# Kernel optimization log

Measured on AMD Instinct MI355X. Metric: run time of the kernel, lower is better.

Reference implementation:

```python
import jax, jax.numpy as jnp
import numpy as np

B, N, D = 2, 2048, 1024
H = 16
HD = D // H  # 64
SCALE = 8.0 / HD  # muP scale = 0.125
EPS = 1e-5


def setup_inputs() -> dict:
    key = jax.random.key(0)
    ks = jax.random.split(key, 7)
    s = 0.02  # realistic init scale for weights
    return {
        "xq": jax.random.normal(ks[0], (B, N, D), jnp.float32),
        "xk": jax.random.normal(ks[1], (B, N, D), jnp.float32),
        "xv": jax.random.normal(ks[2], (B, N, D), jnp.float32),
        "wq": jax.random.normal(ks[3], (D, D), jnp.float32) * s,
        "wk": jax.random.normal(ks[4], (D, D), jnp.float32) * s,
        "wv": jax.random.normal(ks[5], (D, D), jnp.float32) * s,
        "wproj": jax.random.normal(ks[6], (D, D), jnp.float32) * s,
    }


def _layernorm_noaffine(x):
    # Fp32LayerNorm over last dim, no bias / no affine params
    x32 = x.astype(jnp.float32)
    mu = jnp.mean(x32, axis=-1, keepdims=True)
    var = jnp.mean(jnp.square(x32 - mu), axis=-1, keepdims=True)
    return ((x32 - mu) * jax.lax.rsqrt(var + EPS)).astype(x.dtype)


def _heads(x):
    # [B, N, H*HD] -> [B, H, N, HD]
    b, n, _ = x.shape
    return x.reshape(b, n, H, HD).transpose(0, 2, 1, 3)


def reference(xq, xk, xv, wq, wk, wv, wproj):
    # nn.Linear: y = x @ W^T (no bias)
    q = _heads(xq @ wq.T)
    k = _heads(xk @ wk.T)
    v = _heads(xv @ wv.T)
    q = _layernorm_noaffine(q)
    k = _layernorm_noaffine(k)
    # dense attention (score_mod=None, block_mask=None), muP scale
    scores = jnp.einsum("bhqd,bhkd->bhqk", q, k) * SCALE
    attn = jax.nn.softmax(scores, axis=-1)
    o = jnp.einsum("bhqk,bhkd->bhqd", attn, v)
    o = o.transpose(0, 2, 1, 3).reshape(xq.shape[0], xq.shape[1], D)
    return o @ wproj.T
```

## Files before the change

kernel.cpp:

```cpp
#include <hip/hip_runtime.h>

typedef __bf16 bf16x8 __attribute__((ext_vector_type(8)));
typedef float f32x4 __attribute__((ext_vector_type(4)));
typedef float f32x16 __attribute__((ext_vector_type(16)));
typedef unsigned u32x4 __attribute__((ext_vector_type(4)));

#define DEV __device__ __forceinline__
#define L2E 1.44269504f

DEV unsigned short f2bf(float f) {
  unsigned u = __float_as_uint(f);
  u += 0x7fffu + ((u >> 16) & 1u);
  return (unsigned short)(u >> 16);
}
DEV float bf2f(unsigned short h) { return __uint_as_float(((unsigned)h) << 16); }

DEV void gload16(const void* g, void* l) {
  __builtin_amdgcn_global_load_lds((const __attribute__((address_space(1))) void*)g,
                                   (__attribute__((address_space(3))) void*)l, 16, 0, 0);
}

DEV unsigned cvtpk2(float lo, float hi) {
  unsigned r;
  asm("v_cvt_pk_bf16_f32 %0, %1, %2" : "=v"(r) : "v"(lo), "v"(hi));
  return r;
}
DEV void plswap(unsigned& a, unsigned& b) {
  asm volatile("v_permlane32_swap_b32 %0, %1" : "+v"(a), "+v"(b));
}
DEV float ex2(float x) {
  float r;
  asm("v_exp_f32 %0, %1" : "=v"(r) : "v"(x));
  return r;
}
DEV float max3(float a, float b, float c) {
  float r;
  asm("v_max3_f32 %0, %1, %2, %3" : "=v"(r) : "v"(a), "v"(b), "v"(c));
  return r;
}

__global__ __launch_bounds__(256) void cvt7(const float* xq, const float* xk, const float* xv,
                                            const float* wq, const float* wk, const float* wv,
                                            const float* wp, ushort4* xqb, ushort4* xkb,
                                            ushort4* xvb, ushort4* wqb, ushort4* wkb,
                                            ushort4* wvb, ushort4* wpb, int nx4, int nw4) {
  const int y = blockIdx.y;
  const float4* s;
  ushort4* d;
  int n;
  switch (y) {
    case 0: s = (const float4*)xq; d = xqb; n = nx4; break;
    case 1: s = (const float4*)xk; d = xkb; n = nx4; break;
    case 2: s = (const float4*)xv; d = xvb; n = nx4; break;
    case 3: s = (const float4*)wq; d = wqb; n = nw4; break;
    case 4: s = (const float4*)wk; d = wkb; n = nw4; break;
    case 5: s = (const float4*)wv; d = wvb; n = nw4; break;
    default: s = (const float4*)wp; d = wpb; n = nw4; break;
  }
  for (int i = blockIdx.x * 256 + threadIdx.x; i < n; i += gridDim.x * 256) {
    float4 v = s[i];
    ushort4 o;
    o.x = f2bf(v.x); o.y = f2bf(v.y); o.z = f2bf(v.z); o.w = f2bf(v.w);
    d[i] = o;
  }
}

template <bool SWAP>
DEV void gemm_core(const unsigned short* __restrict__ A, const unsigned short* __restrict__ W,
                   char* sA, char* sB, f32x4 acc[4][4], int bm, int bn, int tid) {
  const int w = tid >> 6, lane = tid & 63;
  const int wm = w >> 1, wn = w & 1;
  const char* aB = (const char*)A + ((size_t)(bm * 128 + (lane >> 3)) << 11) +
                   (((lane & 7) ^ (lane >> 3)) << 4);
  const char* bB = (const char*)W + ((size_t)(bn * 128 + (lane >> 3)) << 11) +
                   (((lane & 7) ^ (lane >> 3)) << 4);
  const int ldsBase = w * 1024;

  for (int kt = 0; kt < 16; ++kt) {
    const int ko = kt * 128;
#pragma unroll
    for (int c = 0; c < 4; ++c) {
      gload16(aB + ((size_t)(c * 32 + w * 8) << 11) + ko, sA + c * 4096 + ldsBase);
      gload16(bB + ((size_t)(c * 32 + w * 8) << 11) + ko, sB + c * 4096 + ldsBase);
    }
    __syncthreads();
#pragma unroll
    for (int kk = 0; kk < 2; ++kk) {
      const int ch = ((kk * 4 + (lane >> 4)) ^ (lane & 7)) << 4;
      bf16x8 aF[4], bF[4];
#pragma unroll
      for (int mi = 0; mi < 4; ++mi)
        aF[mi] = *(const bf16x8*)(sA + (wm * 64 + mi * 16 + (lane & 15)) * 128 + ch);
#pragma unroll
      for (int ni = 0; ni < 4; ++ni)
        bF[ni] = *(const bf16x8*)(sB + (wn * 64 + ni * 16 + (lane & 15)) * 128 + ch);
#pragma unroll
      for (int mi = 0; mi < 4; ++mi)
#pragma unroll
        for (int ni = 0; ni < 4; ++ni)
          acc[mi][ni] = SWAP ? __builtin_amdgcn_mfma_f32_16x16x32_bf16(bF[ni], aF[mi],
                                                                       acc[mi][ni], 0, 0, 0)
                             : __builtin_amdgcn_mfma_f32_16x16x32_bf16(aF[mi], bF[ni],
                                                                       acc[mi][ni], 0, 0, 0);
    }
    __syncthreads();
  }
}

__global__ __launch_bounds__(256, 3) void gemm_qkv(
    const unsigned short* __restrict__ xq, const unsigned short* __restrict__ xk,
    const unsigned short* __restrict__ xv, const unsigned short* __restrict__ wq,
    const unsigned short* __restrict__ wk, const unsigned short* __restrict__ wv,
    unsigned short* __restrict__ qh, unsigned short* __restrict__ kh,
    unsigned short* __restrict__ vt) {
  __shared__ char sA[16384], sB[16384];
  const int z = blockIdx.z;
  const int flat = blockIdx.x + (blockIdx.y << 3);
  const int xcd = flat & 7, ii = flat >> 3;
  const int bm = xcd * 4 + (ii >> 3), bn = ii & 7;
  const int tid = threadIdx.x, w = tid >> 6, lane = tid & 63;
  const int wm = w >> 1, wn = w & 1;

  if (z == 2) {
    f32x4 acc[4][4];
#pragma unroll
    for (int i = 0; i < 4; ++i)
#pragma unroll
      for (int j = 0; j < 4; ++j) acc[i][j] = (f32x4){0.f, 0.f, 0.f, 0.f};
    gemm_core<false>(xv, wv, sA, sB, acc, bm, bn, tid);
    const int hb = bn * 2 + wn;
    const int d = (lane & 15);
    const int g0 = bm * 128 + wm * 64 + ((lane >> 4) << 2);
#pragma unroll
    for (int mi = 0; mi < 4; ++mi) {
      const int g = g0 + mi * 16;
      const int b = g >> 11, n0 = g & 2047, tq = n0 >> 6, nn = n0 & 63;
#pragma unroll
      for (int ni = 0; ni < 4; ++ni) {
        const int dd = d + ni * 16;
        char* dst = (char*)vt + (((size_t)((b * 16 + hb) * 32 + tq) * 64 + dd) << 7) +
                    ((nn * 2) ^ ((dd & 7) << 4));
        *(uint2*)dst = make_uint2(cvtpk2(acc[mi][ni][0], acc[mi][ni][1]),
                                  cvtpk2(acc[mi][ni][2], acc[mi][ni][3]));
      }
    }
  } else {
    const unsigned short* A = z == 0 ? xq : xk;
    const unsigned short* W = z == 0 ? wq : wk;
    f32x4 acc[4][4];
#pragma unroll
    for (int i = 0; i < 4; ++i)
#pragma unroll
      for (int j = 0; j < 4; ++j) acc[i][j] = (f32x4){0.f, 0.f, 0.f, 0.f};
    gemm_core<true>(A, W, sA, sB, acc, bm, bn, tid);
    unsigned short* dst = z == 0 ? qh : kh;
    const float osc = z == 0 ? 0.125f * L2E : 1.0f;
    const int h = bn * 2 + wn;
    const int d0b = (lane >> 4) << 3;
#pragma unroll
    for (int mi = 0; mi < 4; ++mi) {
      float s = 0.f, ss = 0.f;
#pragma unroll
      for (int ni = 0; ni < 4; ++ni)
#pragma unroll
        for (int r = 0; r < 4; ++r) {
          const float v = acc[mi][ni][r];
          s += v;
          ss += v * v;
        }
      s += __shfl_xor(s, 16); ss += __shfl_xor(ss, 16);
      s += __shfl_xor(s, 32); ss += __shfl_xor(ss, 32);
      const float mean = s * 0.015625f;
      const float var = ss * 0.015625f - mean * mean;
      const float rstd = rsqrtf(var + 1e-5f) * osc;
      const float mr = mean * rstd;
      const int g = bm * 128 + wm * 64 + mi * 16 + (lane & 15);
      const int b = g >> 11, n = g & 2047;
      const int bh = b * 16 + h, tq = n >> 6, rr = n & 63;
      char* rowp = (char*)dst + (((size_t)(bh * 32 + tq) * 64 + rr) << 7);
      const int swz = (rr & 7) << 4;
#pragma unroll
      for (int ni = 0; ni < 4; ++ni) {
        const unsigned u0 = cvtpk2(fmaf(acc[mi][ni][0], rstd, -mr), fmaf(acc[mi][ni][1], rstd, -mr));
        const unsigned u1 = cvtpk2(fmaf(acc[mi][ni][2], rstd, -mr), fmaf(acc[mi][ni][3], rstd, -mr));
        *(uint2*)(rowp + ((ni * 32 + d0b) ^ swz)) = make_uint2(u0, u1);
      }
    }
  }
}

__global__ __launch_bounds__(256, 3) void gemm_out(const unsigned short* __restrict__ A,
                                                   const unsigned short* __restrict__ Wp,
                                                   float* __restrict__ C) {
  __shared__ char sA[16384], sB[8192];
  const int flat = blockIdx.x + (blockIdx.y << 4);
  const int xcd = flat & 7, ii = flat >> 3;
  const int bm = xcd * 4 + (ii & 3), bn = ii >> 2;
  const int tid = threadIdx.x, w = tid >> 6, lane = tid & 63;
  const int wm = w >> 1, wn = w & 1;
  f32x4 acc[4][2];
#pragma unroll
  for (int i = 0; i < 4; ++i)
#pragma unroll
    for (int j = 0; j < 2; ++j) acc[i][j] = (f32x4){0.f, 0.f, 0.f, 0.f};

  const char* aB = (const char*)A + ((size_t)(bm * 128 + (lane >> 3)) << 11) +
                   (((lane & 7) ^ (lane >> 3)) << 4);
  const char* bB = (const char*)Wp + ((size_t)(bn * 64 + (lane >> 3)) << 11) +
                   (((lane & 7) ^ (lane >> 3)) << 4);
  const int ldsBase = w * 1024;
  for (int kt = 0; kt < 16; ++kt) {
    const int ko = kt * 128;
#pragma unroll
    for (int c = 0; c < 4; ++c)
      gload16(aB + ((size_t)(c * 32 + w * 8) << 11) + ko, sA + c * 4096 + ldsBase);
#pragma unroll
    for (int c = 0; c < 2; ++c)
      gload16(bB + ((size_t)(c * 32 + w * 8) << 11) + ko, sB + c * 4096 + ldsBase);
    __syncthreads();
#pragma unroll
    for (int kk = 0; kk < 2; ++kk) {
      const int ch = ((kk * 4 + (lane >> 4)) ^ (lane & 7)) << 4;
      bf16x8 aF[4], bF[2];
#pragma unroll
      for (int mi = 0; mi < 4; ++mi)
        aF[mi] = *(const bf16x8*)(sA + (wm * 64 + mi * 16 + (lane & 15)) * 128 + ch);
#pragma unroll
      for (int ni = 0; ni < 2; ++ni)
        bF[ni] = *(const bf16x8*)(sB + (wn * 32 + ni * 16 + (lane & 15)) * 128 + ch);
#pragma unroll
      for (int mi = 0; mi < 4; ++mi)
#pragma unroll
        for (int ni = 0; ni < 2; ++ni)
          acc[mi][ni] = __builtin_amdgcn_mfma_f32_16x16x32_bf16(bF[ni], aF[mi], acc[mi][ni], 0, 0, 0);
    }
    __syncthreads();
  }
  const int m0 = bm * 128 + wm * 64 + (lane & 15);
  const int nb = bn * 64 + wn * 32 + ((lane >> 4) << 2);
#pragma unroll
  for (int mi = 0; mi < 4; ++mi)
#pragma unroll
    for (int ni = 0; ni < 2; ++ni) {
      const f32x4 v = acc[mi][ni];
      *(float4*)&C[(size_t)(m0 + mi * 16) * 1024 + nb + ni * 16] =
          make_float4(v[0], v[1], v[2], v[3]);
    }
}

__global__ __launch_bounds__(256, 4) void attn_fused(
    const unsigned short* __restrict__ Qp, const unsigned short* __restrict__ Kp,
    const unsigned short* __restrict__ Vp, unsigned short* __restrict__ Opart,
    float2* __restrict__ ML) {
  const int bid = blockIdx.x;
  const int xcd = bid & 7, idx = bid >> 3;
  const int bh = ((idx & 3) << 3) | xcd;
  const int quarter = (idx >> 2) & 3;
  const int qt = idx >> 4;
  __shared__ char sK[2][8192];
  __shared__ char sV[2][8192];
  const int tid = threadIdx.x, w = tid >> 6, lane = tid & 63;
  const int q5 = lane & 31, hi = lane >> 5;

  const char* qg = (const char*)Qp + ((size_t)bh * 32 + qt * 2) * 8192;
  const char* kg = (const char*)Kp + ((size_t)bh * 32 + quarter * 8) * 8192;
  const char* vg = (const char*)Vp + ((size_t)bh * 32 + quarter * 8) * 8192;

#pragma unroll
  for (int t = 0; t < 4; ++t)
    gload16(qg + (w * 4 + t) * 1024 + lane * 16, (char*)sK + (w * 4 + t) * 1024);
  __syncthreads();
  bf16x8 qf[4];
  {
    const int r128 = w * 32 + q5, tt = r128 >> 6, r = r128 & 63;
#pragma unroll
    for (int dc = 0; dc < 4; ++dc) {
      const int cb = dc * 32 + hi * 16;
      qf[dc] = *(const bf16x8*)((const char*)sK + tt * 8192 + r * 128 + (cb ^ ((r & 7) << 4)));
    }
  }
  __syncthreads();

#pragma unroll
  for (int t = 0; t < 2; ++t) {
    gload16(kg + (w * 2 + t) * 1024 + lane * 16, &sK[0][(w * 2 + t) * 1024]);
    gload16(vg + (w * 2 + t) * 1024 + lane * 16, &sV[0][(w * 2 + t) * 1024]);
  }

  f32x16 o0 = {0,0,0,0,0,0,0,0,0,0,0,0,0,0,0,0};
  f32x16 o1 = {0,0,0,0,0,0,0,0,0,0,0,0,0,0,0,0};
  float m = -1e30f, l = 0.f;

  for (int kt = 0; kt < 8; ++kt) {
    const int cur = kt & 1;
    __syncthreads();
    if (kt < 7) {
#pragma unroll
      for (int t = 0; t < 2; ++t) {
        gload16(kg + (size_t)(kt + 1) * 8192 + (w * 2 + t) * 1024 + lane * 16,
                &sK[cur ^ 1][(w * 2 + t) * 1024]);
        gload16(vg + (size_t)(kt + 1) * 8192 + (w * 2 + t) * 1024 + lane * 16,
                &sV[cur ^ 1][(w * 2 + t) * 1024]);
      }
    }
    f32x16 s0 = {0,0,0,0,0,0,0,0,0,0,0,0,0,0,0,0};
    f32x16 s1 = {0,0,0,0,0,0,0,0,0,0,0,0,0,0,0,0};
    __builtin_amdgcn_s_setprio(1);
#pragma unroll
    for (int dc = 0; dc < 4; ++dc) {
      const int cb = dc * 32 + hi * 16;
      const int ra = q5, rb = 32 + q5;
      bf16x8 kf0 = *(const bf16x8*)(&sK[cur][ra * 128 + (cb ^ ((ra & 7) << 4))]);
      bf16x8 kf1 = *(const bf16x8*)(&sK[cur][rb * 128 + (cb ^ ((rb & 7) << 4))]);
      s0 = __builtin_amdgcn_mfma_f32_32x32x16_bf16(kf0, qf[dc], s0, 0, 0, 0);
      s1 = __builtin_amdgcn_mfma_f32_32x32x16_bf16(kf1, qf[dc], s1, 0, 0, 0);
    }
    __builtin_amdgcn_s_setprio(0);
    float tt[12];
#pragma unroll
    for (int r = 0; r < 10; ++r) {
      const float a = (3 * r) < 16 ? s0[(3 * r) & 15] : s1[(3 * r) & 15];
      const float b = (3 * r + 1) < 16 ? s0[(3 * r + 1) & 15] : s1[(3 * r + 1) & 15];
      const float c = (3 * r + 2) < 16 ? s0[(3 * r + 2) & 15] : s1[(3 * r + 2) & 15];
      tt[r] = max3(a, b, c);
    }
    tt[10] = s1[14]; tt[11] = s1[15];
    tt[0] = max3(tt[0], tt[1], tt[2]);
    tt[1] = max3(tt[3], tt[4], tt[5]);
    tt[2] = max3(tt[6], tt[7], tt[8]);
    tt[3] = max3(tt[9], tt[10], tt[11]);
    const float loc = fmaxf(max3(tt[0], tt[1], tt[2]), tt[3]);
    const float mx = fmaxf(loc, __shfl_xor(loc, 32));
    if (__any(mx > m + 8.f)) {
      const float mn = fmaxf(m, mx);
      const float corr = ex2(m - mn);
      l *= corr;
#pragma unroll
      for (int r = 0; r < 16; ++r) { o0[r] *= corr; o1[r] *= corr; }
      m = mn;
    }
    const float nm = -m;
    unsigned pk[4][4];
    float rs = 0.f;
#define DO_CHUNK(c, SV, B)                                      \
  {                                                             \
    float p0 = ex2(SV[B + 0] + nm);                             \
    float p1 = ex2(SV[B + 1] + nm);                             \
    float p2 = ex2(SV[B + 2] + nm);                             \
    float p3 = ex2(SV[B + 3] + nm);                             \
    float p4 = ex2(SV[B + 4] + nm);                             \
    float p5 = ex2(SV[B + 5] + nm);                             \
    float p6 = ex2(SV[B + 6] + nm);                             \
    float p7 = ex2(SV[B + 7] + nm);                             \
    rs += ((p0 + p1) + (p2 + p3)) + ((p4 + p5) + (p6 + p7));    \
    unsigned a0 = cvtpk2(p0, p1), a1 = cvtpk2(p2, p3);          \
    unsigned b0 = cvtpk2(p4, p5), b1 = cvtpk2(p6, p7);          \
    plswap(a0, b0);                                             \
    plswap(a1, b1);                                             \
    pk[c][0] = a0; pk[c][1] = a1; pk[c][2] = b0; pk[c][3] = b1; \
  }
    DO_CHUNK(0, s0, 0)
    DO_CHUNK(1, s0, 8)
    DO_CHUNK(2, s1, 0)
    DO_CHUNK(3, s1, 8)
#undef DO_CHUNK
    rs += __shfl_xor(rs, 32);
    l += rs;
    __builtin_amdgcn_s_setprio(1);
#pragma unroll
    for (int kk = 0; kk < 4; ++kk) {
      const int cb = kk * 32 + hi * 16;
      const int ra = q5, rb = 32 + q5;
      bf16x8 vf0 = *(const bf16x8*)(&sV[cur][ra * 128 + (cb ^ ((ra & 7) << 4))]);
      bf16x8 vf1 = *(const bf16x8*)(&sV[cur][rb * 128 + (cb ^ ((rb & 7) << 4))]);
      u32x4 pw = {pk[kk][0], pk[kk][1], pk[kk][2], pk[kk][3]};
      bf16x8 pb = __builtin_bit_cast(bf16x8, pw);
      o0 = __builtin_amdgcn_mfma_f32_32x32x16_bf16(vf0, pb, o0, 0, 0, 0);
      o1 = __builtin_amdgcn_mfma_f32_32x32x16_bf16(vf1, pb, o1, 0, 0, 0);
    }
    __builtin_amdgcn_s_setprio(0);
  }

  const float invl = 1.f / l;
  const int q = qt * 128 + w * 32 + q5;
  const size_t prow = (size_t)(quarter * 32 + bh) * 2048 + q;
  unsigned short* ob = Opart + prow * 64;
#pragma unroll
  for (int g = 0; g < 4; ++g) {
    unsigned d0 = cvtpk2(o0[4 * g + 0] * invl, o0[4 * g + 1] * invl);
    unsigned d1 = cvtpk2(o0[4 * g + 2] * invl, o0[4 * g + 3] * invl);
    *(uint2*)(ob + 8 * g + 4 * hi) = make_uint2(d0, d1);
    unsigned e0 = cvtpk2(o1[4 * g + 0] * invl, o1[4 * g + 1] * invl);
    unsigned e1 = cvtpk2(o1[4 * g + 2] * invl, o1[4 * g + 3] * invl);
    *(uint2*)(ob + 32 + 8 * g + 4 * hi) = make_uint2(e0, e1);
  }
  if (hi == 0) ML[prow] = make_float2(m, l);
}

__global__ __launch_bounds__(256) void attn_merge(const unsigned short* __restrict__ Op,
                                                  const float2* __restrict__ ML,
                                                  unsigned short* __restrict__ O) {
  const int gid = blockIdx.x * 256 + threadIdx.x;
  const int row = gid >> 3, sub = gid & 7;
  float2 ml[4];
  float mm = -1e30f;
#pragma unroll
  for (int p = 0; p < 4; ++p) {
    ml[p] = ML[p * 65536 + row];
    mm = fmaxf(mm, ml[p].x);
  }
  float wgt[4], wsum = 0.f;
#pragma unroll
  for (int p = 0; p < 4; ++p) {
    wgt[p] = ml[p].y * ex2(ml[p].x - mm);
    wsum += wgt[p];
  }
  const float inv = 1.f / wsum;
  float r[8] = {0.f, 0.f, 0.f, 0.f, 0.f, 0.f, 0.f, 0.f};
#pragma unroll
  for (int p = 0; p < 4; ++p) {
    const uint4 a = *(const uint4*)(Op + ((size_t)(p * 65536) + row) * 64 + sub * 8);
    const unsigned av[4] = {a.x, a.y, a.z, a.w};
#pragma unroll
    for (int j = 0; j < 4; ++j) {
      r[2 * j] += wgt[p] * bf2f((unsigned short)(av[j] & 0xffff));
      r[2 * j + 1] += wgt[p] * bf2f((unsigned short)(av[j] >> 16));
    }
  }
  unsigned ov[4];
#pragma unroll
  for (int j = 0; j < 4; ++j)
    ov[j] = cvtpk2(r[2 * j] * inv, r[2 * j + 1] * inv);
  const int bh = row >> 11, q = row & 2047, bb = bh >> 4, h = bh & 15;
  *(uint4*)(O + ((size_t)(bb * 2048 + q) * 1024 + h * 64 + sub * 8)) =
      make_uint4(ov[0], ov[1], ov[2], ov[3]);
}

extern "C" void kernel_launch(void* const* d_in, const int* in_sizes, int n_in,
                              void* d_out, int out_size, void* d_ws, size_t ws_size,
                              hipStream_t stream) {
  const float* xq = (const float*)d_in[0];
  const float* xk = (const float*)d_in[1];
  const float* xv = (const float*)d_in[2];
  const float* wq = (const float*)d_in[3];
  const float* wk = (const float*)d_in[4];
  const float* wv = (const float*)d_in[5];
  const float* wp = (const float*)d_in[6];

  const size_t NX = 4194304;
  const size_t NW = 1048576;
  unsigned short* base = (unsigned short*)d_ws;
  unsigned short* xqb = base;
  unsigned short* xkb = base + NX;
  unsigned short* xvb = base + 2 * NX;
  unsigned short* wqb = base + 3 * NX;
  unsigned short* wkb = wqb + NW;
  unsigned short* wvb = wkb + NW;
  unsigned short* wpb = base + 3 * NX + 4 * NW;
  unsigned short* qh = wpb + NW;
  unsigned short* kh = qh + NX;
  unsigned short* vt = kh + NX;
  unsigned short* obf = vt + NX;
  float2* ml = (float2*)(obf + NX);
  unsigned short* opart = base;

  cvt7<<<dim3(512, 7), 256, 0, stream>>>(xq, xk, xv, wq, wk, wv, wp, (ushort4*)xqb,
                                         (ushort4*)xkb, (ushort4*)xvb, (ushort4*)wqb,
                                         (ushort4*)wkb, (ushort4*)wvb, (ushort4*)wpb,
                                         (int)(NX / 4), (int)(NW / 4));

  gemm_qkv<<<dim3(8, 32, 3), 256, 0, stream>>>(xqb, xkb, xvb, wqb, wkb, wvb, qh, kh, vt);

  attn_fused<<<2048, 256, 0, stream>>>(qh, kh, vt, opart, ml);
  attn_merge<<<2048, 256, 0, stream>>>(opart, ml, obf);

  gemm_out<<<dim3(16, 32), 256, 0, stream>>>(obf, wpb, (float*)d_out);
}
```

Measured before the change: 129.1 us.

## Double attention query tile per block and swap K/V fragment loads via permlane

```diff
diff --git a/kernel.cpp b/kernel.cpp
--- a/kernel.cpp
+++ b/kernel.cpp
@@ -37,6 +37,18 @@
   float r;
   asm("v_max3_f32 %0, %1, %2, %3" : "=v"(r) : "v"(a), "v"(b), "v"(c));
   return r;
+}
+
+DEV void read2swap(const char* base, int c0, int lane, bf16x8& f0, bf16x8& f1) {
+  const int swz = (lane & 7) << 4;
+  const u32x4 a = *(const u32x4*)(base + lane * 128 + (c0 ^ swz));
+  const u32x4 b = *(const u32x4*)(base + lane * 128 + ((c0 + 16) ^ swz));
+  unsigned a0 = a[0], a1 = a[1], a2 = a[2], a3 = a[3];
+  unsigned b0 = b[0], b1 = b[1], b2 = b[2], b3 = b[3];
+  plswap(a0, b0); plswap(a1, b1); plswap(a2, b2); plswap(a3, b3);
+  const u32x4 ra = {a0, a1, a2, a3}, rb = {b0, b1, b2, b3};
+  f0 = __builtin_bit_cast(bf16x8, ra);
+  f1 = __builtin_bit_cast(bf16x8, rb);
 }
 
 __global__ __launch_bounds__(256) void cvt7(const float* xq, const float* xk, const float* xv,
@@ -248,153 +260,178 @@
     }
 }
 
-__global__ __launch_bounds__(256, 4) void attn_fused(
+__global__ __launch_bounds__(256, 2) void attn_fused(
     const unsigned short* __restrict__ Qp, const unsigned short* __restrict__ Kp,
     const unsigned short* __restrict__ Vp, unsigned short* __restrict__ Opart,
     float2* __restrict__ ML) {
   const int bid = blockIdx.x;
   const int xcd = bid & 7, idx = bid >> 3;
   const int bh = ((idx & 3) << 3) | xcd;
-  const int quarter = (idx >> 2) & 3;
-  const int qt = idx >> 4;
-  __shared__ char sK[2][8192];
-  __shared__ char sV[2][8192];
+  const int rest = idx >> 2;
+  const int quarter = rest & 3;
+  const int qt = rest >> 2;
+  __shared__ char smem[32768];
   const int tid = threadIdx.x, w = tid >> 6, lane = tid & 63;
   const int q5 = lane & 31, hi = lane >> 5;
 
-  const char* qg = (const char*)Qp + ((size_t)bh * 32 + qt * 2) * 8192;
+  const char* qg = (const char*)Qp + ((size_t)bh * 32 + qt * 4) * 8192;
   const char* kg = (const char*)Kp + ((size_t)bh * 32 + quarter * 8) * 8192;
   const char* vg = (const char*)Vp + ((size_t)bh * 32 + quarter * 8) * 8192;
 
 #pragma unroll
-  for (int t = 0; t < 4; ++t)
-    gload16(qg + (w * 4 + t) * 1024 + lane * 16, (char*)sK + (w * 4 + t) * 1024);
+  for (int t = 0; t < 8; ++t)
+    gload16(qg + (w * 8 + t) * 1024 + lane * 16, smem + (w * 8 + t) * 1024);
   __syncthreads();
-  bf16x8 qf[4];
-  {
-    const int r128 = w * 32 + q5, tt = r128 >> 6, r = r128 & 63;
+  bf16x8 qf[2][4];
+#pragma unroll
+  for (int g = 0; g < 2; ++g) {
+    const int qrow = w * 64 + g * 32 + q5;
+    const int tt = qrow >> 6, r = qrow & 63;
 #pragma unroll
     for (int dc = 0; dc < 4; ++dc) {
       const int cb = dc * 32 + hi * 16;
-      qf[dc] = *(const bf16x8*)((const char*)sK + tt * 8192 + r * 128 + (cb ^ ((r & 7) << 4)));
+      qf[g][dc] = *(const bf16x8*)(smem + tt * 8192 + r * 128 + (cb ^ ((r & 7) << 4)));
     }
   }
   __syncthreads();
 
 #pragma unroll
   for (int t = 0; t < 2; ++t) {
-    gload16(kg + (w * 2 + t) * 1024 + lane * 16, &sK[0][(w * 2 + t) * 1024]);
-    gload16(vg + (w * 2 + t) * 1024 + lane * 16, &sV[0][(w * 2 + t) * 1024]);
-  }
-
-  f32x16 o0 = {0,0,0,0,0,0,0,0,0,0,0,0,0,0,0,0};
-  f32x16 o1 = {0,0,0,0,0,0,0,0,0,0,0,0,0,0,0,0};
-  float m = -1e30f, l = 0.f;
+    gload16(kg + (w * 2 + t) * 1024 + lane * 16, smem + (w * 2 + t) * 1024);
+    gload16(vg + (w * 2 + t) * 1024 + lane * 16, smem + 16384 + (w * 2 + t) * 1024);
+  }
+
+  f32x16 o[2][2];
+#pragma unroll
+  for (int g = 0; g < 2; ++g)
+#pragma unroll
+    for (int h = 0; h < 2; ++h) o[g][h] = (f32x16){0,0,0,0,0,0,0,0,0,0,0,0,0,0,0,0};
+  float m[2] = {-1e30f, -1e30f}, l[2] = {0.f, 0.f};
 
   for (int kt = 0; kt < 8; ++kt) {
     const int cur = kt & 1;
+    const int kOff = cur * 8192;
+    const int vOff = 16384 + cur * 8192;
     __syncthreads();
     if (kt < 7) {
+      const int kN = (cur ^ 1) * 8192, vN = 16384 + (cur ^ 1) * 8192;
 #pragma unroll
       for (int t = 0; t < 2; ++t) {
         gload16(kg + (size_t)(kt + 1) * 8192 + (w * 2 + t) * 1024 + lane * 16,
-                &sK[cur ^ 1][(w * 2 + t) * 1024]);
+                smem + kN + (w * 2 + t) * 1024);
         gload16(vg + (size_t)(kt + 1) * 8192 + (w * 2 + t) * 1024 + lane * 16,
-                &sV[cur ^ 1][(w * 2 + t) * 1024]);
+                smem + vN + (w * 2 + t) * 1024);
       }
     }
-    f32x16 s0 = {0,0,0,0,0,0,0,0,0,0,0,0,0,0,0,0};
-    f32x16 s1 = {0,0,0,0,0,0,0,0,0,0,0,0,0,0,0,0};
+    f32x16 s[2][2];
+#pragma unroll
+    for (int g = 0; g < 2; ++g)
+#pragma unroll
+      for (int h = 0; h < 2; ++h) s[g][h] = (f32x16){0,0,0,0,0,0,0,0,0,0,0,0,0,0,0,0};
     __builtin_amdgcn_s_setprio(1);
 #pragma unroll
     for (int dc = 0; dc < 4; ++dc) {
-      const int cb = dc * 32 + hi * 16;
-      const int ra = q5, rb = 32 + q5;
-      bf16x8 kf0 = *(const bf16x8*)(&sK[cur][ra * 128 + (cb ^ ((ra & 7) << 4))]);
-      bf16x8 kf1 = *(const bf16x8*)(&sK[cur][rb * 128 + (cb ^ ((rb & 7) << 4))]);
-      s0 = __builtin_amdgcn_mfma_f32_32x32x16_bf16(kf0, qf[dc], s0, 0, 0, 0);
-      s1 = __builtin_amdgcn_mfma_f32_32x32x16_bf16(kf1, qf[dc], s1, 0, 0, 0);
+      bf16x8 kf0, kf1;
+      read2swap(smem + kOff, dc * 32, lane, kf0, kf1);
+      s[0][0] = __builtin_amdgcn_mfma_f32_32x32x16_bf16(kf0, qf[0][dc], s[0][0], 0, 0, 0);
+      s[0][1] = __builtin_amdgcn_mfma_f32_32x32x16_bf16(kf1, qf[0][dc], s[0][1], 0, 0, 0);
+      s[1][0] = __builtin_amdgcn_mfma_f32_32x32x16_bf16(kf0, qf[1][dc], s[1][0], 0, 0, 0);
+      s[1][1] = __builtin_amdgcn_mfma_f32_32x32x16_bf16(kf1, qf[1][dc], s[1][1], 0, 0, 0);
     }
     __builtin_amdgcn_s_setprio(0);
-    float tt[12];
-#pragma unroll
-    for (int r = 0; r < 10; ++r) {
-      const float a = (3 * r) < 16 ? s0[(3 * r) & 15] : s1[(3 * r) & 15];
-      const float b = (3 * r + 1) < 16 ? s0[(3 * r + 1) & 15] : s1[(3 * r + 1) & 15];
-      const float c = (3 * r + 2) < 16 ? s0[(3 * r + 2) & 15] : s1[(3 * r + 2) & 15];
-      tt[r] = max3(a, b, c);
-    }
-    tt[10] = s1[14]; tt[11] = s1[15];
-    tt[0] = max3(tt[0], tt[1], tt[2]);
-    tt[1] = max3(tt[3], tt[4], tt[5]);
-    tt[2] = max3(tt[6], tt[7], tt[8]);
-    tt[3] = max3(tt[9], tt[10], tt[11]);
-    const float loc = fmaxf(max3(tt[0], tt[1], tt[2]), tt[3]);
-    const float mx = fmaxf(loc, __shfl_xor(loc, 32));
-    if (__any(mx > m + 8.f)) {
-      const float mn = fmaxf(m, mx);
-      const float corr = ex2(m - mn);
-      l *= corr;
-#pragma unroll
-      for (int r = 0; r < 16; ++r) { o0[r] *= corr; o1[r] *= corr; }
-      m = mn;
-    }
-    const float nm = -m;
-    unsigned pk[4][4];
-    float rs = 0.f;
-#define DO_CHUNK(c, SV, B)                                      \
-  {                                                             \
-    float p0 = ex2(SV[B + 0] + nm);                             \
-    float p1 = ex2(SV[B + 1] + nm);                             \
-    float p2 = ex2(SV[B + 2] + nm);                             \
-    float p3 = ex2(SV[B + 3] + nm);                             \
-    float p4 = ex2(SV[B + 4] + nm);                             \
-    float p5 = ex2(SV[B + 5] + nm);                             \
-    float p6 = ex2(SV[B + 6] + nm);                             \
-    float p7 = ex2(SV[B + 7] + nm);                             \
-    rs += ((p0 + p1) + (p2 + p3)) + ((p4 + p5) + (p6 + p7));    \
-    unsigned a0 = cvtpk2(p0, p1), a1 = cvtpk2(p2, p3);          \
-    unsigned b0 = cvtpk2(p4, p5), b1 = cvtpk2(p6, p7);          \
-    plswap(a0, b0);                                             \
-    plswap(a1, b1);                                             \
-    pk[c][0] = a0; pk[c][1] = a1; pk[c][2] = b0; pk[c][3] = b1; \
-  }
-    DO_CHUNK(0, s0, 0)
-    DO_CHUNK(1, s0, 8)
-    DO_CHUNK(2, s1, 0)
-    DO_CHUNK(3, s1, 8)
+    float mx[2];
+#pragma unroll
+    for (int g = 0; g < 2; ++g) {
+      float tt[12];
+#pragma unroll
+      for (int r = 0; r < 10; ++r) {
+        const float a = (3 * r) < 16 ? s[g][0][(3 * r) & 15] : s[g][1][(3 * r) & 15];
+        const float b = (3 * r + 1) < 16 ? s[g][0][(3 * r + 1) & 15] : s[g][1][(3 * r + 1) & 15];
+        const float c = (3 * r + 2) < 16 ? s[g][0][(3 * r + 2) & 15] : s[g][1][(3 * r + 2) & 15];
+        tt[r] = max3(a, b, c);
+      }
+      tt[10] = s[g][1][14]; tt[11] = s[g][1][15];
+      tt[0] = max3(tt[0], tt[1], tt[2]);
+      tt[1] = max3(tt[3], tt[4], tt[5]);
+      tt[2] = max3(tt[6], tt[7], tt[8]);
+      tt[3] = max3(tt[9], tt[10], tt[11]);
+      const float loc = fmaxf(max3(tt[0], tt[1], tt[2]), tt[3]);
+      mx[g] = fmaxf(loc, __shfl_xor(loc, 32));
+    }
+    if (__any((mx[0] > m[0] + 8.f) || (mx[1] > m[1] + 8.f))) {
+#pragma unroll
+      for (int g = 0; g < 2; ++g) {
+        const float mn = fmaxf(m[g], mx[g]);
+        const float corr = ex2(m[g] - mn);
+        l[g] *= corr;
+#pragma unroll
+        for (int r = 0; r < 16; ++r) { o[g][0][r] *= corr; o[g][1][r] *= corr; }
+        m[g] = mn;
+      }
+    }
+    unsigned pk[2][4][4];
+#pragma unroll
+    for (int g = 0; g < 2; ++g) {
+      const float nm = -m[g];
+      float rs = 0.f;
+#define DO_CHUNK(c, SV, B)                                         \
+  {                                                                \
+    float p0 = ex2(SV[B + 0] + nm);                                \
+    float p1 = ex2(SV[B + 1] + nm);                                \
+    float p2 = ex2(SV[B + 2] + nm);                                \
+    float p3 = ex2(SV[B + 3] + nm);                                \
+    float p4 = ex2(SV[B + 4] + nm);                                \
+    float p5 = ex2(SV[B + 5] + nm);                                \
+    float p6 = ex2(SV[B + 6] + nm);                                \
+    float p7 = ex2(SV[B + 7] + nm);                                \
+    rs += ((p0 + p1) + (p2 + p3)) + ((p4 + p5) + (p6 + p7));       \
+    unsigned a0 = cvtpk2(p0, p1), a1 = cvtpk2(p2, p3);             \
+    unsigned b0 = cvtpk2(p4, p5), b1 = cvtpk2(p6, p7);             \
+    plswap(a0, b0);                                                \
+    plswap(a1, b1);                                                \
+    pk[g][c][0] = a0; pk[g][c][1] = a1; pk[g][c][2] = b0; pk[g][c][3] = b1; \
+  }
+      DO_CHUNK(0, s[g][0], 0)
+      DO_CHUNK(1, s[g][0], 8)
+      DO_CHUNK(2, s[g][1], 0)
+      DO_CHUNK(3, s[g][1], 8)
 #undef DO_CHUNK
-    rs += __shfl_xor(rs, 32);
-    l += rs;
+      rs += __shfl_xor(rs, 32);
+      l[g] += rs;
+    }
     __builtin_amdgcn_s_setprio(1);
 #pragma unroll
     for (int kk = 0; kk < 4; ++kk) {
-      const int cb = kk * 32 + hi * 16;
-      const int ra = q5, rb = 32 + q5;
-      bf16x8 vf0 = *(const bf16x8*)(&sV[cur][ra * 128 + (cb ^ ((ra & 7) << 4))]);
-      bf16x8 vf1 = *(const bf16x8*)(&sV[cur][rb * 128 + (cb ^ ((rb & 7) << 4))]);
-      u32x4 pw = {pk[kk][0], pk[kk][1], pk[kk][2], pk[kk][3]};
-      bf16x8 pb = __builtin_bit_cast(bf16x8, pw);
-      o0 = __builtin_amdgcn_mfma_f32_32x32x16_bf16(vf0, pb, o0, 0, 0, 0);
-      o1 = __builtin_amdgcn_mfma_f32_32x32x16_bf16(vf1, pb, o1, 0, 0, 0);
+      bf16x8 vf0, vf1;
+      read2swap(smem + vOff, kk * 32, lane, vf0, vf1);
+#pragma unroll
+      for (int g = 0; g < 2; ++g) {
+        const u32x4 pw = {pk[g][kk][0], pk[g][kk][1], pk[g][kk][2], pk[g][kk][3]};
+        const bf16x8 pb = __builtin_bit_cast(bf16x8, pw);
+        o[g][0] = __builtin_amdgcn_mfma_f32_32x32x16_bf16(vf0, pb, o[g][0], 0, 0, 0);
+        o[g][1] = __builtin_amdgcn_mfma_f32_32x32x16_bf16(vf1, pb, o[g][1], 0, 0, 0);
+      }
     }
     __builtin_amdgcn_s_setprio(0);
   }
 
-  const float invl = 1.f / l;
-  const int q = qt * 128 + w * 32 + q5;
-  const size_t prow = (size_t)(quarter * 32 + bh) * 2048 + q;
-  unsigned short* ob = Opart + prow * 64;
-#pragma unroll
-  for (int g = 0; g < 4; ++g) {
-    unsigned d0 = cvtpk2(o0[4 * g + 0] * invl, o0[4 * g + 1] * invl);
-    unsigned d1 = cvtpk2(o0[4 * g + 2] * invl, o0[4 * g + 3] * invl);
-    *(uint2*)(ob + 8 * g + 4 * hi) = make_uint2(d0, d1);
-    unsigned e0 = cvtpk2(o1[4 * g + 0] * invl, o1[4 * g + 1] * invl);
-    unsigned e1 = cvtpk2(o1[4 * g + 2] * invl, o1[4 * g + 3] * invl);
-    *(uint2*)(ob + 32 + 8 * g + 4 * hi) = make_uint2(e0, e1);
-  }
-  if (hi == 0) ML[prow] = make_float2(m, l);
+#pragma unroll
+  for (int g = 0; g < 2; ++g) {
+    const float invl = 1.f / l[g];
+    const int q = qt * 256 + w * 64 + g * 32 + q5;
+    const size_t prow = (size_t)(quarter * 32 + bh) * 2048 + q;
+    unsigned short* ob = Opart + prow * 64;
+#pragma unroll
+    for (int g4 = 0; g4 < 4; ++g4) {
+      unsigned d0 = cvtpk2(o[g][0][4 * g4 + 0] * invl, o[g][0][4 * g4 + 1] * invl);
+      unsigned d1 = cvtpk2(o[g][0][4 * g4 + 2] * invl, o[g][0][4 * g4 + 3] * invl);
+      *(uint2*)(ob + 8 * g4 + 4 * hi) = make_uint2(d0, d1);
+      unsigned e0 = cvtpk2(o[g][1][4 * g4 + 0] * invl, o[g][1][4 * g4 + 1] * invl);
+      unsigned e1 = cvtpk2(o[g][1][4 * g4 + 2] * invl, o[g][1][4 * g4 + 3] * invl);
+      *(uint2*)(ob + 32 + 8 * g4 + 4 * hi) = make_uint2(e0, e1);
+    }
+    if (hi == 0) ML[prow] = make_float2(m[g], l[g]);
+  }
 }
 
 __global__ __launch_bounds__(256) void attn_merge(const unsigned short* __restrict__ Op,
@@ -471,7 +508,7 @@
 
   gemm_qkv<<<dim3(8, 32, 3), 256, 0, stream>>>(xqb, xkb, xvb, wqb, wkb, wvb, qh, kh, vt);
 
-  attn_fused<<<2048, 256, 0, stream>>>(qh, kh, vt, opart, ml);
+  attn_fused<<<1024, 256, 0, stream>>>(qh, kh, vt, opart, ml);
   attn_merge<<<2048, 256, 0, stream>>>(opart, ml, obf);
 
   gemm_out<<<dim3(16, 32), 256, 0, stream>>>(obf, wpb, (float*)d_out);
```

Result: slower. 135.1 us (+4.7%).

## Store Q/K/V tiles in MFMA-fragment order for linear LDS reads

Applied to the files above, without the earlier changes.

```diff
diff --git a/kernel.cpp b/kernel.cpp
--- a/kernel.cpp
+++ b/kernel.cpp
@@ -38,6 +38,7 @@
   asm("v_max3_f32 %0, %1, %2, %3" : "=v"(r) : "v"(a), "v"(b), "v"(c));
   return r;
 }
+
 
 __global__ __launch_bounds__(256) void cvt7(const float* xq, const float* xk, const float* xv,
                                             const float* wq, const float* wk, const float* wv,
@@ -138,8 +139,9 @@
 #pragma unroll
       for (int ni = 0; ni < 4; ++ni) {
         const int dd = d + ni * 16;
-        char* dst = (char*)vt + (((size_t)((b * 16 + hb) * 32 + tq) * 64 + dd) << 7) +
-                    ((nn * 2) ^ ((dd & 7) << 4));
+        char* dst = (char*)vt + ((size_t)((b * 16 + hb) * 32 + tq) << 13) +
+                    (((nn >> 4) * 2 + (dd >> 5)) << 10) + (((nn >> 3) & 1) << 9) +
+                    ((dd & 31) << 4) + ((nn & 7) << 1);
         *(uint2*)dst = make_uint2(cvtpk2(acc[mi][ni][0], acc[mi][ni][1]),
                                   cvtpk2(acc[mi][ni][2], acc[mi][ni][3]));
       }
@@ -156,7 +158,8 @@
     unsigned short* dst = z == 0 ? qh : kh;
     const float osc = z == 0 ? 0.125f * L2E : 1.0f;
     const int h = bn * 2 + wn;
-    const int d0b = (lane >> 4) << 3;
+    const int hiK = lane >> 5;
+    const int low8 = ((lane >> 4) & 1) << 3;
 #pragma unroll
     for (int mi = 0; mi < 4; ++mi) {
       float s = 0.f, ss = 0.f;
@@ -177,13 +180,13 @@
       const int g = bm * 128 + wm * 64 + mi * 16 + (lane & 15);
       const int b = g >> 11, n = g & 2047;
       const int bh = b * 16 + h, tq = n >> 6, rr = n & 63;
-      char* rowp = (char*)dst + (((size_t)(bh * 32 + tq) * 64 + rr) << 7);
-      const int swz = (rr & 7) << 4;
+      char* tbase = (char*)dst + ((size_t)(bh * 32 + tq) << 13);
 #pragma unroll
       for (int ni = 0; ni < 4; ++ni) {
         const unsigned u0 = cvtpk2(fmaf(acc[mi][ni][0], rstd, -mr), fmaf(acc[mi][ni][1], rstd, -mr));
         const unsigned u1 = cvtpk2(fmaf(acc[mi][ni][2], rstd, -mr), fmaf(acc[mi][ni][3], rstd, -mr));
-        *(uint2*)(rowp + ((ni * 32 + d0b) ^ swz)) = make_uint2(u0, u1);
+        char* p = tbase + ((ni * 2 + (rr >> 5)) << 10) + (hiK << 9) + ((rr & 31) << 4) + low8;
+        *(uint2*)p = make_uint2(u0, u1);
       }
     }
   }
@@ -255,36 +258,34 @@
   const int bid = blockIdx.x;
   const int xcd = bid & 7, idx = bid >> 3;
   const int bh = ((idx & 3) << 3) | xcd;
-  const int quarter = (idx >> 2) & 3;
-  const int qt = idx >> 4;
-  __shared__ char sK[2][8192];
-  __shared__ char sV[2][8192];
+  const int rest = idx >> 2;
+  const int quarter = rest & 3;
+  const int qt = rest >> 2;
+  __shared__ char smem[32768];
   const int tid = threadIdx.x, w = tid >> 6, lane = tid & 63;
   const int q5 = lane & 31, hi = lane >> 5;
 
-  const char* qg = (const char*)Qp + ((size_t)bh * 32 + qt * 2) * 8192;
-  const char* kg = (const char*)Kp + ((size_t)bh * 32 + quarter * 8) * 8192;
-  const char* vg = (const char*)Vp + ((size_t)bh * 32 + quarter * 8) * 8192;
+  const char* qg = (const char*)Qp + ((size_t)(bh * 32 + qt * 2) << 13);
+  const char* kg = (const char*)Kp + ((size_t)(bh * 32 + quarter * 8) << 13);
+  const char* vg = (const char*)Vp + ((size_t)(bh * 32 + quarter * 8) << 13);
 
 #pragma unroll
   for (int t = 0; t < 4; ++t)
-    gload16(qg + (w * 4 + t) * 1024 + lane * 16, (char*)sK + (w * 4 + t) * 1024);
+    gload16(qg + (w * 4 + t) * 1024 + lane * 16, smem + (w * 4 + t) * 1024);
   __syncthreads();
   bf16x8 qf[4];
   {
-    const int r128 = w * 32 + q5, tt = r128 >> 6, r = r128 & 63;
-#pragma unroll
-    for (int dc = 0; dc < 4; ++dc) {
-      const int cb = dc * 32 + hi * 16;
-      qf[dc] = *(const bf16x8*)((const char*)sK + tt * 8192 + r * 128 + (cb ^ ((r & 7) << 4)));
-    }
+    const int qbase = (w >> 1) * 8192 + ((w & 1) << 10);
+#pragma unroll
+    for (int dc = 0; dc < 4; ++dc)
+      qf[dc] = *(const bf16x8*)(smem + qbase + (dc << 11) + lane * 16);
   }
   __syncthreads();
 
 #pragma unroll
   for (int t = 0; t < 2; ++t) {
-    gload16(kg + (w * 2 + t) * 1024 + lane * 16, &sK[0][(w * 2 + t) * 1024]);
-    gload16(vg + (w * 2 + t) * 1024 + lane * 16, &sV[0][(w * 2 + t) * 1024]);
+    gload16(kg + (w * 2 + t) * 1024 + lane * 16, smem + (w * 2 + t) * 1024);
+    gload16(vg + (w * 2 + t) * 1024 + lane * 16, smem + 16384 + (w * 2 + t) * 1024);
   }
 
   f32x16 o0 = {0,0,0,0,0,0,0,0,0,0,0,0,0,0,0,0};
@@ -293,14 +294,17 @@
 
   for (int kt = 0; kt < 8; ++kt) {
     const int cur = kt & 1;
+    const int kOff = cur * 8192;
+    const int vOff = 16384 + cur * 8192;
     __syncthreads();
     if (kt < 7) {
+      const int kN = (cur ^ 1) * 8192, vN = 16384 + (cur ^ 1) * 8192;
 #pragma unroll
       for (int t = 0; t < 2; ++t) {
         gload16(kg + (size_t)(kt + 1) * 8192 + (w * 2 + t) * 1024 + lane * 16,
-                &sK[cur ^ 1][(w * 2 + t) * 1024]);
+                smem + kN + (w * 2 + t) * 1024);
         gload16(vg + (size_t)(kt + 1) * 8192 + (w * 2 + t) * 1024 + lane * 16,
-                &sV[cur ^ 1][(w * 2 + t) * 1024]);
+                smem + vN + (w * 2 + t) * 1024);
       }
     }
     f32x16 s0 = {0,0,0,0,0,0,0,0,0,0,0,0,0,0,0,0};
@@ -308,10 +312,8 @@
     __builtin_amdgcn_s_setprio(1);
 #pragma unroll
     for (int dc = 0; dc < 4; ++dc) {
-      const int cb = dc * 32 + hi * 16;
-      const int ra = q5, rb = 32 + q5;
-      bf16x8 kf0 = *(const bf16x8*)(&sK[cur][ra * 128 + (cb ^ ((ra & 7) << 4))]);
-      bf16x8 kf1 = *(const bf16x8*)(&sK[cur][rb * 128 + (cb ^ ((rb & 7) << 4))]);
+      const bf16x8 kf0 = *(const bf16x8*)(smem + kOff + (dc << 11) + lane * 16);
+      const bf16x8 kf1 = *(const bf16x8*)(smem + kOff + (dc << 11) + 1024 + lane * 16);
       s0 = __builtin_amdgcn_mfma_f32_32x32x16_bf16(kf0, qf[dc], s0, 0, 0, 0);
       s1 = __builtin_amdgcn_mfma_f32_32x32x16_bf16(kf1, qf[dc], s1, 0, 0, 0);
     }
@@ -369,12 +371,10 @@
     __builtin_amdgcn_s_setprio(1);
 #pragma unroll
     for (int kk = 0; kk < 4; ++kk) {
-      const int cb = kk * 32 + hi * 16;
-      const int ra = q5, rb = 32 + q5;
-      bf16x8 vf0 = *(const bf16x8*)(&sV[cur][ra * 128 + (cb ^ ((ra & 7) << 4))]);
-      bf16x8 vf1 = *(const bf16x8*)(&sV[cur][rb * 128 + (cb ^ ((rb & 7) << 4))]);
-      u32x4 pw = {pk[kk][0], pk[kk][1], pk[kk][2], pk[kk][3]};
-      bf16x8 pb = __builtin_bit_cast(bf16x8, pw);
+      const bf16x8 vf0 = *(const bf16x8*)(smem + vOff + (kk << 11) + lane * 16);
+      const bf16x8 vf1 = *(const bf16x8*)(smem + vOff + (kk << 11) + 1024 + lane * 16);
+      const u32x4 pw = {pk[kk][0], pk[kk][1], pk[kk][2], pk[kk][3]};
+      const bf16x8 pb = __builtin_bit_cast(bf16x8, pw);
       o0 = __builtin_amdgcn_mfma_f32_32x32x16_bf16(vf0, pb, o0, 0, 0, 0);
       o1 = __builtin_amdgcn_mfma_f32_32x32x16_bf16(vf1, pb, o1, 0, 0, 0);
     }
```

After: 126.5 us. -2.0%, faster.
